# Kernel optimization log

Hardware: AMD Instinct MI355X
Metric: run time of the kernel (lower is better)

The kernel has to match this reference:

```python
import jax, jax.numpy as jnp
import numpy as np
import math

B, T, D, H, QS, VS, V, HID = 4096, 16, 32, 4, 64, 64, 65, 2048


def _sinusoidal(block_size, dmodel):
    pe = np.zeros((block_size, dmodel), dtype=np.float32)
    pos = np.arange(block_size)[:, None].astype(np.float32)
    i = np.arange(dmodel // 2).astype(np.float32)
    denom = 10000.0 ** (2.0 * i / dmodel)
    pe[:, 0::2] = np.sin(pos / denom)
    pe[:, 1::2] = np.cos(pos / denom)
    return jnp.asarray(pe)


def setup_inputs() -> dict:
    key = jax.random.key(0)
    ks = jax.random.split(key, 20)
    n = lambda k, s: jax.random.normal(k, s, jnp.float32) * 0.05
    return {
        "x": jax.random.randint(ks[0], (B, T), 0, V, dtype=jnp.int32),
        "emb": n(ks[1], (V, D)),
        "pos": _sinusoidal(T, D),
        "Wq": n(ks[2], (2, H, D, QS)), "bq": n(ks[3], (2, H, QS)),
        "Wk": n(ks[4], (2, H, D, QS)), "bk": n(ks[5], (2, H, QS)),
        "Wv": n(ks[6], (2, H, D, VS)), "bv": n(ks[7], (2, H, VS)),
        "Wo": n(ks[8], (2, H * VS, D)), "bo": n(ks[9], (2, D)),
        "ga": jnp.ones((2, D), jnp.float32), "ba": jnp.zeros((2, D), jnp.float32),
        "W1": n(ks[10], (2, D, HID)), "b1": n(ks[11], (2, HID)),
        "W2": n(ks[12], (2, HID, D)), "b2": n(ks[13], (2, D)),
        "gm": jnp.ones((2, D), jnp.float32), "bm": jnp.zeros((2, D), jnp.float32),
        "Wf": n(ks[14], (D, V)), "bf": n(ks[15], (V,)),
    }


def _ln(x, g, b, eps=1e-5):
    m = jnp.mean(x, axis=-1, keepdims=True)
    v = jnp.mean((x - m) ** 2, axis=-1, keepdims=True)
    return (x - m) * jax.lax.rsqrt(v + eps) * g + b


def reference(x, emb, pos, Wq, bq, Wk, bk, Wv, bv, Wo, bo, ga, ba,
              W1, b1, W2, b2, gm, bm, Wf, bf):
    # embed + sinusoidal pos, scaled by sqrt(dmodel) (as in source)
    h = (emb[x] + pos) * math.sqrt(D)  # [B,T,D]
    mask = jnp.tril(jnp.ones((T, T), dtype=bool))
    for l in range(2):
        # all H heads at once: [B,H,T,QS]
        q = jnp.einsum('btd,hdq->bhtq', h, Wq[l]) + bq[l][:, None, :]
        k = jnp.einsum('btd,hdq->bhtq', h, Wk[l]) + bk[l][:, None, :]
        v = jnp.einsum('btd,hdv->bhtv', h, Wv[l]) + bv[l][:, None, :]
        s = jnp.einsum('bhtq,bhsq->bhts', q, k) / math.sqrt(QS)
        s = jnp.where(mask, s, -jnp.inf)
        a = jax.nn.softmax(s, axis=-1)
        o = jnp.einsum('bhts,bhsv->bhtv', a, v)
        o = o.transpose(0, 2, 1, 3).reshape(h.shape[0], T, H * VS)  # concat heads
        o = o @ Wo[l] + bo[l]
        h = _ln(o + h, ga[l], ba[l])
        m = jax.nn.relu(h @ W1[l] + b1[l]) @ W2[l] + b2[l]
        h = _ln(h + m, gm[l], bm[l])
    return h @ Wf + bf  # logits [B,T,V]
```

## Files before the change

kernel.cpp:

```cpp
#include <hip/hip_runtime.h>

typedef __bf16 bf16;
typedef __bf16 bf16x4 __attribute__((ext_vector_type(4)));
typedef __bf16 bf16x8 __attribute__((ext_vector_type(8)));
typedef short  s16x4  __attribute__((ext_vector_type(4)));
typedef float  f32x4  __attribute__((ext_vector_type(4)));

#define VOC 65

#define LDS_FENCE() asm volatile("s_waitcnt lgkmcnt(0)" ::: "memory")

#define WS_WQ 0
#define WS_WK 16384
#define WS_WV 32768
#define WS_WO 49152
#define WS_W1 65536
#define WS_W2 196608
#define WS_WF 327680

__global__ void transpose_f32bf16_k(const float* __restrict__ src, bf16* __restrict__ dst,
                                    int batch, int R, int C) {
  int i = blockIdx.x * blockDim.x + threadIdx.x;
  int total = batch * R * C;
  if (i >= total) return;
  int b = i / (R * C);
  int rc = i - b * (R * C);
  int r = rc / C;
  int c = rc - r * C;
  dst[(b * C + c) * R + r] = (bf16)src[i];
}

__global__ void prep_wf_k(const float* __restrict__ wf, bf16* __restrict__ dst) {
  int i = blockIdx.x * blockDim.x + threadIdx.x;
  if (i >= 80 * 32) return;
  int c = i >> 5, r = i & 31;
  dst[i] = (c < VOC) ? (bf16)wf[r * VOC + c] : (bf16)0.0f;
}


#define MFMA32(a,b,c) __builtin_amdgcn_mfma_f32_16x16x32_bf16((a),(b),(c),0,0,0)

static __device__ __forceinline__ f32x4 MFMA16(bf16x4 a, bf16x4 b, f32x4 c) {
  return __builtin_amdgcn_mfma_f32_16x16x16bf16_1k(
      __builtin_bit_cast(s16x4, a), __builtin_bit_cast(s16x4, b), c, 0, 0, 0);
}

static __device__ __forceinline__ f32x4 splat4(float v) {
  f32x4 s; s[0] = v; s[1] = v; s[2] = v; s[3] = v; return s;
}

#define NS 4

__global__ __launch_bounds__(128)
void xformer_k(const int* __restrict__ x, const float* __restrict__ emb, const float* __restrict__ pos,
               const float* __restrict__ bq, const float* __restrict__ bk, const float* __restrict__ bv,
               const float* __restrict__ bo, const float* __restrict__ ga, const float* __restrict__ ba,
               const float* __restrict__ b1, const float* __restrict__ b2,
               const float* __restrict__ gm, const float* __restrict__ bm,
               const float* __restrict__ bfin,
               const bf16* __restrict__ ws, float* __restrict__ out)
{
  __shared__ bf16 hbnc[2][NS][16][40];
  const int tid  = threadIdx.x;
  const int wv   = tid >> 6;
  const int lane = tid & 63;
  const int lo   = lane & 15;
  const int hi   = lane >> 4;
  const int seq0 = blockIdx.x * (2*NS) + wv * NS;

  const bf16* wqT = ws + WS_WQ;
  const bf16* wkT = ws + WS_WK;
  const bf16* wvT = ws + WS_WV;
  const bf16* woT = ws + WS_WO;
  const bf16* w1T = ws + WS_W1;
  const bf16* w2T = ws + WS_W2;
  const bf16* wfT = ws + WS_WF;

  const f32x4 fz = {0.f, 0.f, 0.f, 0.f};

  bf16x8 bh[NS];
  bf16x4 hD0[NS], hD1[NS];

  #pragma unroll
  for (int si = 0; si < NS; ++si) {
    const int s = seq0 + si;
    int idl = x[s*16 + lo];
    idl = idl < 0 ? 0 : (idl >= VOC ? VOC - 1 : idl);
    f32x4 e0 = *(const f32x4*)(emb + idl*32 + hi*8);
    f32x4 e1 = *(const f32x4*)(emb + idl*32 + hi*8 + 4);
    f32x4 p0 = *(const f32x4*)(pos + lo*32 + hi*8);
    f32x4 p1 = *(const f32x4*)(pos + lo*32 + hi*8 + 4);
    bf16x8 hv;
    #pragma unroll
    for (int j = 0; j < 4; ++j) {
      hv[j]   = (bf16)((e0[j] + p0[j]) * 5.656854249492381f);
      hv[4+j] = (bf16)((e1[j] + p1[j]) * 5.656854249492381f);
    }
    bh[si] = hv;
    bf16x4 d0, d1;
    #pragma unroll
    for (int r = 0; r < 4; ++r) {
      int tr = hi*4 + r;
      int idr = x[s*16 + tr];
      idr = idr < 0 ? 0 : (idr >= VOC ? VOC - 1 : idr);
      d0[r] = (bf16)((emb[idr*32 + lo]      + pos[tr*32 + lo])      * 5.656854249492381f);
      d1[r] = (bf16)((emb[idr*32 + 16 + lo] + pos[tr*32 + 16 + lo]) * 5.656854249492381f);
    }
    hD0[si] = d0; hD1[si] = d1;
  }

  for (int l = 0; l < 2; ++l) {
    f32x4 accO[NS][2];
    {
      float bo0 = bo[l*32 + lo], bo1 = bo[l*32 + 16 + lo];
      #pragma unroll
      for (int si = 0; si < NS; ++si) { accO[si][0] = splat4(bo0); accO[si][1] = splat4(bo1); }
    }
    #pragma unroll
    for (int hh = 0; hh < 4; ++hh) {
      const int hb = (l*4 + hh) * 64;
      f32x4 sf[NS];
      #pragma unroll
      for (int si = 0; si < NS; ++si) sf[si] = fz;
      #pragma unroll
      for (int nt = 0; nt < 4; ++nt) {
        const int wofs = (hb + nt*16 + lo)*32 + hi*8;
        bf16x8 wq8 = *(const bf16x8*)(wqT + wofs);
        bf16x8 wk8 = *(const bf16x8*)(wkT + wofs);
        f32x4 bq4 = *(const f32x4*)(bq + hb + nt*16 + hi*4);
        f32x4 bk4 = *(const f32x4*)(bk + hb + nt*16 + hi*4);
        #pragma unroll
        for (int si = 0; si < NS; ++si) {
          f32x4 dq = MFMA32(wq8, bh[si], bq4);
          f32x4 dk = MFMA32(wk8, bh[si], bk4);
          bf16x4 pq, pk;
          #pragma unroll
          for (int r = 0; r < 4; ++r) {
            pq[r] = (bf16)dq[r];
            pk[r] = (bf16)dk[r];
          }
          sf[si] = MFMA16(pk, pq, sf[si]);
        }
      }
      bf16x4 pp[NS];
      #pragma unroll
      for (int si = 0; si < NS; ++si) {
        float e[4], mx = -3.0e4f, sm = 0.f;
        #pragma unroll
        for (int r = 0; r < 4; ++r) {
          int key = hi*4 + r;
          e[r] = (key <= lo) ? sf[si][r] * 0.125f : -3.0e4f;
          mx = fmaxf(mx, e[r]);
        }
        mx = fmaxf(mx, __shfl_xor(mx, 16));
        mx = fmaxf(mx, __shfl_xor(mx, 32));
        #pragma unroll
        for (int r = 0; r < 4; ++r) { e[r] = __expf(e[r] - mx); sm += e[r]; }
        sm += __shfl_xor(sm, 16);
        sm += __shfl_xor(sm, 32);
        float inv = 1.0f / sm;
        bf16x4 p4;
        #pragma unroll
        for (int r = 0; r < 4; ++r) p4[r] = (bf16)(e[r] * inv);
        pp[si] = p4;
      }
      #pragma unroll
      for (int nt = 0; nt < 4; ++nt) {
        bf16x8 wv8 = *(const bf16x8*)(wvT + (hb + nt*16 + lo)*32 + hi*8);
        f32x4 bv4 = splat4(bv[hb + nt*16 + lo]);
        bf16x4 wo4[2];
        #pragma unroll
        for (int n2 = 0; n2 < 2; ++n2)
          wo4[n2] = *(const bf16x4*)(woT + (l*32 + n2*16 + lo)*256 + hh*64 + nt*16 + hi*4);
        #pragma unroll
        for (int si = 0; si < NS; ++si) {
          f32x4 dv = MFMA32(bh[si], wv8, bv4);
          bf16x4 vz;
          #pragma unroll
          for (int r = 0; r < 4; ++r) vz[r] = (bf16)dv[r];
          f32x4 o = MFMA16(vz, pp[si], fz);
          bf16x4 oz;
          #pragma unroll
          for (int r = 0; r < 4; ++r) oz[r] = (bf16)o[r];
          #pragma unroll
          for (int n2 = 0; n2 < 2; ++n2)
            accO[si][n2] = MFMA16(oz, wo4[n2], accO[si][n2]);
        }
      }
    }
    {
      float g0 = ga[l*32 + lo], g1 = ga[l*32 + 16 + lo];
      float a0 = ba[l*32 + lo], a1 = ba[l*32 + 16 + lo];
      #pragma unroll
      for (int si = 0; si < NS; ++si) {
        bf16x4 nh0, nh1;
        #pragma unroll
        for (int r = 0; r < 4; ++r) {
          float v0 = accO[si][0][r] + (float)hD0[si][r];
          float v1 = accO[si][1][r] + (float)hD1[si][r];
          float s1 = v0 + v1, s2 = v0*v0 + v1*v1;
          s1 += __shfl_xor(s1, 1); s2 += __shfl_xor(s2, 1);
          s1 += __shfl_xor(s1, 2); s2 += __shfl_xor(s2, 2);
          s1 += __shfl_xor(s1, 4); s2 += __shfl_xor(s2, 4);
          s1 += __shfl_xor(s1, 8); s2 += __shfl_xor(s2, 8);
          float mean = s1 * (1.f/32.f);
          float var  = s2 * (1.f/32.f) - mean*mean;
          float rs   = rsqrtf(fabsf(var) + 1e-5f);
          float h0 = (v0 - mean)*rs*g0 + a0;
          float h1 = (v1 - mean)*rs*g1 + a1;
          nh0[r] = (bf16)h0; nh1[r] = (bf16)h1;
          hbnc[wv][si][hi*4 + r][lo]      = (bf16)h0;
          hbnc[wv][si][hi*4 + r][16 + lo] = (bf16)h1;
        }
        hD0[si] = nh0; hD1[si] = nh1;
      }
      LDS_FENCE();
      #pragma unroll
      for (int si = 0; si < NS; ++si)
        bh[si] = *(const bf16x8*)(&hbnc[wv][si][lo][hi*8]);
      LDS_FENCE();
    }
    f32x4 acc2[NS][2];
    {
      float b20 = b2[l*32 + lo], b21 = b2[l*32 + 16 + lo];
      #pragma unroll
      for (int si = 0; si < NS; ++si) { acc2[si][0] = splat4(b20); acc2[si][1] = splat4(b21); }
    }
    const bf16* w1l = w1T + l*65536;
    const bf16* w2l = w2T + l*65536;
    const float* b1l = b1 + l*2048;
    bf16x8 A1[2]; bf16x4 A2[2][2]; f32x4 Ab[2];
    bf16x8 B1[2]; bf16x4 B2[2][2]; f32x4 Bb[2];
    #pragma unroll
    for (int c = 0; c < 2; ++c) {
      A1[c] = *(const bf16x8*)(w1l + (c*16 + lo)*32 + hi*8);
      Ab[c] = *(const f32x4*)(b1l + c*16 + hi*4);
      B1[c] = *(const bf16x8*)(w1l + (32 + c*16 + lo)*32 + hi*8);
      Bb[c] = *(const f32x4*)(b1l + 32 + c*16 + hi*4);
      #pragma unroll
      for (int n2 = 0; n2 < 2; ++n2) {
        A2[c][n2] = *(const bf16x4*)(w2l + (n2*16 + lo)*2048 + c*16 + hi*4);
        B2[c][n2] = *(const bf16x4*)(w2l + (n2*16 + lo)*2048 + 32 + c*16 + hi*4);
      }
    }
    for (int kk = 0; kk < 64; kk += 2) {
      {
        const int k2 = ((kk + 2) & 63) * 32;
        bf16x8 n1[2]; bf16x4 n2v[2][2]; f32x4 nb[2];
        #pragma unroll
        for (int c = 0; c < 2; ++c) {
          n1[c] = *(const bf16x8*)(w1l + (k2 + c*16 + lo)*32 + hi*8);
          nb[c] = *(const f32x4*)(b1l + k2 + c*16 + hi*4);
          #pragma unroll
          for (int n2 = 0; n2 < 2; ++n2)
            n2v[c][n2] = *(const bf16x4*)(w2l + (n2*16 + lo)*2048 + k2 + c*16 + hi*4);
        }
        #pragma unroll
        for (int c = 0; c < 2; ++c) {
          #pragma unroll
          for (int si = 0; si < NS; ++si) {
            f32x4 d = MFMA32(A1[c], bh[si], Ab[c]);
            bf16x4 mz;
            #pragma unroll
            for (int r = 0; r < 4; ++r) mz[r] = (bf16)fmaxf(d[r], 0.f);
            acc2[si][0] = MFMA16(mz, A2[c][0], acc2[si][0]);
            acc2[si][1] = MFMA16(mz, A2[c][1], acc2[si][1]);
          }
        }
        #pragma unroll
        for (int c = 0; c < 2; ++c) {
          A1[c] = n1[c]; Ab[c] = nb[c];
          A2[c][0] = n2v[c][0]; A2[c][1] = n2v[c][1];
        }
      }
      {
        const int k3 = ((kk + 3) & 63) * 32;
        bf16x8 n1[2]; bf16x4 n2v[2][2]; f32x4 nb[2];
        #pragma unroll
        for (int c = 0; c < 2; ++c) {
          n1[c] = *(const bf16x8*)(w1l + (k3 + c*16 + lo)*32 + hi*8);
          nb[c] = *(const f32x4*)(b1l + k3 + c*16 + hi*4);
          #pragma unroll
          for (int n2 = 0; n2 < 2; ++n2)
            n2v[c][n2] = *(const bf16x4*)(w2l + (n2*16 + lo)*2048 + k3 + c*16 + hi*4);
        }
        #pragma unroll
        for (int c = 0; c < 2; ++c) {
          #pragma unroll
          for (int si = 0; si < NS; ++si) {
            f32x4 d = MFMA32(B1[c], bh[si], Bb[c]);
            bf16x4 mz;
            #pragma unroll
            for (int r = 0; r < 4; ++r) mz[r] = (bf16)fmaxf(d[r], 0.f);
            acc2[si][0] = MFMA16(mz, B2[c][0], acc2[si][0]);
            acc2[si][1] = MFMA16(mz, B2[c][1], acc2[si][1]);
          }
        }
        #pragma unroll
        for (int c = 0; c < 2; ++c) {
          B1[c] = n1[c]; Bb[c] = nb[c];
          B2[c][0] = n2v[c][0]; B2[c][1] = n2v[c][1];
        }
      }
    }
    {
      float g0 = gm[l*32 + lo], g1 = gm[l*32 + 16 + lo];
      float a0 = bm[l*32 + lo], a1 = bm[l*32 + 16 + lo];
      #pragma unroll
      for (int si = 0; si < NS; ++si) {
        bf16x4 nh0, nh1;
        #pragma unroll
        for (int r = 0; r < 4; ++r) {
          float v0 = acc2[si][0][r] + (float)hD0[si][r];
          float v1 = acc2[si][1][r] + (float)hD1[si][r];
          float s1 = v0 + v1, s2 = v0*v0 + v1*v1;
          s1 += __shfl_xor(s1, 1); s2 += __shfl_xor(s2, 1);
          s1 += __shfl_xor(s1, 2); s2 += __shfl_xor(s2, 2);
          s1 += __shfl_xor(s1, 4); s2 += __shfl_xor(s2, 4);
          s1 += __shfl_xor(s1, 8); s2 += __shfl_xor(s2, 8);
          float mean = s1 * (1.f/32.f);
          float var  = s2 * (1.f/32.f) - mean*mean;
          float rs   = rsqrtf(fabsf(var) + 1e-5f);
          float h0 = (v0 - mean)*rs*g0 + a0;
          float h1 = (v1 - mean)*rs*g1 + a1;
          nh0[r] = (bf16)h0; nh1[r] = (bf16)h1;
          hbnc[wv][si][hi*4 + r][lo]      = (bf16)h0;
          hbnc[wv][si][hi*4 + r][16 + lo] = (bf16)h1;
        }
        hD0[si] = nh0; hD1[si] = nh1;
      }
      LDS_FENCE();
      #pragma unroll
      for (int si = 0; si < NS; ++si)
        bh[si] = *(const bf16x8*)(&hbnc[wv][si][lo][hi*8]);
      LDS_FENCE();
    }
  }

  #pragma unroll
  for (int si = 0; si < NS; ++si) {
    const int s = seq0 + si;
    bf16x8 a = bh[si];
    #pragma unroll
    for (int nt = 0; nt < 5; ++nt) {
      int col = nt*16 + lo;
      f32x4 cb = splat4((col < VOC) ? bfin[col] : 0.f);
      bf16x8 w = *(const bf16x8*)(wfT + (nt*16 + lo)*32 + hi*8);
      f32x4 d = MFMA32(a, w, cb);
      if (col < VOC) {
        #pragma unroll
        for (int r = 0; r < 4; ++r)
          out[(s*16 + hi*4 + r)*VOC + col] = d[r];
      }
    }
  }
}

extern "C" void kernel_launch(void* const* d_in, const int* in_sizes, int n_in,
                              void* d_out, int out_size, void* d_ws, size_t ws_size,
                              hipStream_t stream) {
  const int*   x   = (const int*)d_in[0];
  const float* emb = (const float*)d_in[1];
  const float* pos = (const float*)d_in[2];
  const float* Wq  = (const float*)d_in[3];
  const float* bq  = (const float*)d_in[4];
  const float* Wk  = (const float*)d_in[5];
  const float* bk  = (const float*)d_in[6];
  const float* Wv  = (const float*)d_in[7];
  const float* bv  = (const float*)d_in[8];
  const float* Wo  = (const float*)d_in[9];
  const float* bo  = (const float*)d_in[10];
  const float* ga  = (const float*)d_in[11];
  const float* ba  = (const float*)d_in[12];
  const float* W1  = (const float*)d_in[13];
  const float* b1  = (const float*)d_in[14];
  const float* W2  = (const float*)d_in[15];
  const float* b2  = (const float*)d_in[16];
  const float* gm  = (const float*)d_in[17];
  const float* bm  = (const float*)d_in[18];
  const float* Wf  = (const float*)d_in[19];
  const float* bfin= (const float*)d_in[20];

  bf16* ws = (bf16*)d_ws;

  transpose_f32bf16_k<<<64, 256, 0, stream>>>(Wq, ws + WS_WQ, 8, 32, 64);
  transpose_f32bf16_k<<<64, 256, 0, stream>>>(Wk, ws + WS_WK, 8, 32, 64);
  transpose_f32bf16_k<<<64, 256, 0, stream>>>(Wv, ws + WS_WV, 8, 32, 64);
  transpose_f32bf16_k<<<64, 256, 0, stream>>>(Wo, ws + WS_WO, 2, 256, 32);
  transpose_f32bf16_k<<<512, 256, 0, stream>>>(W1, ws + WS_W1, 2, 32, 2048);
  transpose_f32bf16_k<<<512, 256, 0, stream>>>(W2, ws + WS_W2, 2, 2048, 32);
  prep_wf_k<<<10, 256, 0, stream>>>(Wf, ws + WS_WF);

  xformer_k<<<512, 128, 0, stream>>>(x, emb, pos, bq, bk, bv, bo, ga, ba,
                                     b1, b2, gm, bm, bfin,
                                     ws, (float*)d_out);
}
```

Baseline: 145.2 us.

## Use K=32 MFMA for QK scores and FFN down-projection with permuted W2

```diff
diff --git a/kernel.cpp b/kernel.cpp
--- a/kernel.cpp
+++ b/kernel.cpp
@@ -30,6 +30,19 @@
   dst[(b * C + c) * R + r] = (bf16)src[i];
 }
 
+__global__ void prep_w2perm_k(const float* __restrict__ src, bf16* __restrict__ dst) {
+  int i = blockIdx.x * blockDim.x + threadIdx.x;
+  if (i >= 2 * 2048 * 32) return;
+  int l   = i >> 16;
+  int rem = i & 65535;
+  int hid = rem >> 5;
+  int out = rem & 31;
+  int h5 = hid & 31;
+  int c  = (h5 >> 4) & 1, hh = (h5 >> 2) & 3, r = h5 & 3;
+  int hid_p = (hid & ~31) | (hh << 3) | (c << 2) | r;
+  dst[(l*32 + out)*2048 + hid_p] = (bf16)src[i];
+}
+
 __global__ void prep_wf_k(const float* __restrict__ wf, bf16* __restrict__ dst) {
   int i = blockIdx.x * blockDim.x + threadIdx.x;
   if (i >= 80 * 32) return;
@@ -50,6 +63,25 @@
 }
 
 #define NS 4
+
+struct FSet {
+  bf16x8 w10, w11;
+  bf16x8 w20, w21;
+  f32x4  b0, b1;
+};
+
+static __device__ __forceinline__ FSet load_fset(const bf16* w1l, const bf16* w2l,
+                                                 const float* b1l, int kk, int lo, int hi) {
+  FSet S;
+  const int hb = (kk & 63) * 32;
+  S.w10 = *(const bf16x8*)(w1l + (hb + lo)*32 + hi*8);
+  S.w11 = *(const bf16x8*)(w1l + (hb + 16 + lo)*32 + hi*8);
+  S.b0  = *(const f32x4*)(b1l + hb + hi*4);
+  S.b1  = *(const f32x4*)(b1l + hb + 16 + hi*4);
+  S.w20 = *(const bf16x8*)(w2l + (lo)*2048 + hb + hi*8);
+  S.w21 = *(const bf16x8*)(w2l + (16 + lo)*2048 + hb + hi*8);
+  return S;
+}
 
 __global__ __launch_bounds__(128)
 void xformer_k(const int* __restrict__ x, const float* __restrict__ emb, const float* __restrict__ pos,
@@ -123,24 +155,30 @@
       #pragma unroll
       for (int si = 0; si < NS; ++si) sf[si] = fz;
       #pragma unroll
-      for (int nt = 0; nt < 4; ++nt) {
-        const int wofs = (hb + nt*16 + lo)*32 + hi*8;
-        bf16x8 wq8 = *(const bf16x8*)(wqT + wofs);
-        bf16x8 wk8 = *(const bf16x8*)(wkT + wofs);
-        f32x4 bq4 = *(const f32x4*)(bq + hb + nt*16 + hi*4);
-        f32x4 bk4 = *(const f32x4*)(bk + hb + nt*16 + hi*4);
-        #pragma unroll
-        for (int si = 0; si < NS; ++si) {
-          f32x4 dq = MFMA32(wq8, bh[si], bq4);
-          f32x4 dk = MFMA32(wk8, bh[si], bk4);
-          bf16x4 pq, pk;
+      for (int ntp = 0; ntp < 2; ++ntp) {
+        bf16x8 pq8[NS], pk8[NS];
+        #pragma unroll
+        for (int c = 0; c < 2; ++c) {
+          const int nt = ntp*2 + c;
+          const int wofs = (hb + nt*16 + lo)*32 + hi*8;
+          bf16x8 wq8 = *(const bf16x8*)(wqT + wofs);
+          bf16x8 wk8 = *(const bf16x8*)(wkT + wofs);
+          f32x4 bq4 = *(const f32x4*)(bq + hb + nt*16 + hi*4);
+          f32x4 bk4 = *(const f32x4*)(bk + hb + nt*16 + hi*4);
           #pragma unroll
-          for (int r = 0; r < 4; ++r) {
-            pq[r] = (bf16)dq[r];
-            pk[r] = (bf16)dk[r];
+          for (int si = 0; si < NS; ++si) {
+            f32x4 dq = MFMA32(wq8, bh[si], bq4);
+            f32x4 dk = MFMA32(wk8, bh[si], bk4);
+            #pragma unroll
+            for (int r = 0; r < 4; ++r) {
+              pq8[si][c*4 + r] = (bf16)dq[r];
+              pk8[si][c*4 + r] = (bf16)dk[r];
+            }
           }
-          sf[si] = MFMA16(pk, pq, sf[si]);
-        }
+        }
+        #pragma unroll
+        for (int si = 0; si < NS; ++si)
+          sf[si] = MFMA32(pk8[si], pq8[si], sf[si]);
       }
       bf16x4 pp[NS];
       #pragma unroll
@@ -229,79 +267,25 @@
     const bf16* w1l = w1T + l*65536;
     const bf16* w2l = w2T + l*65536;
     const float* b1l = b1 + l*2048;
-    bf16x8 A1[2]; bf16x4 A2[2][2]; f32x4 Ab[2];
-    bf16x8 B1[2]; bf16x4 B2[2][2]; f32x4 Bb[2];
-    #pragma unroll
-    for (int c = 0; c < 2; ++c) {
-      A1[c] = *(const bf16x8*)(w1l + (c*16 + lo)*32 + hi*8);
-      Ab[c] = *(const f32x4*)(b1l + c*16 + hi*4);
-      B1[c] = *(const bf16x8*)(w1l + (32 + c*16 + lo)*32 + hi*8);
-      Bb[c] = *(const f32x4*)(b1l + 32 + c*16 + hi*4);
-      #pragma unroll
-      for (int n2 = 0; n2 < 2; ++n2) {
-        A2[c][n2] = *(const bf16x4*)(w2l + (n2*16 + lo)*2048 + c*16 + hi*4);
-        B2[c][n2] = *(const bf16x4*)(w2l + (n2*16 + lo)*2048 + 32 + c*16 + hi*4);
-      }
-    }
-    for (int kk = 0; kk < 64; kk += 2) {
-      {
-        const int k2 = ((kk + 2) & 63) * 32;
-        bf16x8 n1[2]; bf16x4 n2v[2][2]; f32x4 nb[2];
-        #pragma unroll
-        for (int c = 0; c < 2; ++c) {
-          n1[c] = *(const bf16x8*)(w1l + (k2 + c*16 + lo)*32 + hi*8);
-          nb[c] = *(const f32x4*)(b1l + k2 + c*16 + hi*4);
-          #pragma unroll
-          for (int n2 = 0; n2 < 2; ++n2)
-            n2v[c][n2] = *(const bf16x4*)(w2l + (n2*16 + lo)*2048 + k2 + c*16 + hi*4);
-        }
-        #pragma unroll
-        for (int c = 0; c < 2; ++c) {
-          #pragma unroll
-          for (int si = 0; si < NS; ++si) {
-            f32x4 d = MFMA32(A1[c], bh[si], Ab[c]);
-            bf16x4 mz;
-            #pragma unroll
-            for (int r = 0; r < 4; ++r) mz[r] = (bf16)fmaxf(d[r], 0.f);
-            acc2[si][0] = MFMA16(mz, A2[c][0], acc2[si][0]);
-            acc2[si][1] = MFMA16(mz, A2[c][1], acc2[si][1]);
-          }
-        }
-        #pragma unroll
-        for (int c = 0; c < 2; ++c) {
-          A1[c] = n1[c]; Ab[c] = nb[c];
-          A2[c][0] = n2v[c][0]; A2[c][1] = n2v[c][1];
-        }
-      }
-      {
-        const int k3 = ((kk + 3) & 63) * 32;
-        bf16x8 n1[2]; bf16x4 n2v[2][2]; f32x4 nb[2];
-        #pragma unroll
-        for (int c = 0; c < 2; ++c) {
-          n1[c] = *(const bf16x8*)(w1l + (k3 + c*16 + lo)*32 + hi*8);
-          nb[c] = *(const f32x4*)(b1l + k3 + c*16 + hi*4);
-          #pragma unroll
-          for (int n2 = 0; n2 < 2; ++n2)
-            n2v[c][n2] = *(const bf16x4*)(w2l + (n2*16 + lo)*2048 + k3 + c*16 + hi*4);
-        }
-        #pragma unroll
-        for (int c = 0; c < 2; ++c) {
-          #pragma unroll
-          for (int si = 0; si < NS; ++si) {
-            f32x4 d = MFMA32(B1[c], bh[si], Bb[c]);
-            bf16x4 mz;
-            #pragma unroll
-            for (int r = 0; r < 4; ++r) mz[r] = (bf16)fmaxf(d[r], 0.f);
-            acc2[si][0] = MFMA16(mz, B2[c][0], acc2[si][0]);
-            acc2[si][1] = MFMA16(mz, B2[c][1], acc2[si][1]);
-          }
-        }
-        #pragma unroll
-        for (int c = 0; c < 2; ++c) {
-          B1[c] = n1[c]; Bb[c] = nb[c];
-          B2[c][0] = n2v[c][0]; B2[c][1] = n2v[c][1];
-        }
-      }
+    FSet SA = load_fset(w1l, w2l, b1l, 0, lo, hi);
+    FSet SB = load_fset(w1l, w2l, b1l, 1, lo, hi);
+    #pragma unroll 2
+    for (int kk = 0; kk < 64; ++kk) {
+      FSet N = load_fset(w1l, w2l, b1l, kk + 2, lo, hi);
+      #pragma unroll
+      for (int si = 0; si < NS; ++si) {
+        f32x4 d0 = MFMA32(SA.w10, bh[si], SA.b0);
+        f32x4 d1 = MFMA32(SA.w11, bh[si], SA.b1);
+        bf16x8 m8;
+        #pragma unroll
+        for (int r = 0; r < 4; ++r) {
+          m8[r]     = (bf16)fmaxf(d0[r], 0.f);
+          m8[4 + r] = (bf16)fmaxf(d1[r], 0.f);
+        }
+        acc2[si][0] = MFMA32(m8, SA.w20, acc2[si][0]);
+        acc2[si][1] = MFMA32(m8, SA.w21, acc2[si][1]);
+      }
+      SA = SB; SB = N;
     }
     {
       float g0 = gm[l*32 + lo], g1 = gm[l*32 + 16 + lo];
@@ -388,7 +372,7 @@
   transpose_f32bf16_k<<<64, 256, 0, stream>>>(Wv, ws + WS_WV, 8, 32, 64);
   transpose_f32bf16_k<<<64, 256, 0, stream>>>(Wo, ws + WS_WO, 2, 256, 32);
   transpose_f32bf16_k<<<512, 256, 0, stream>>>(W1, ws + WS_W1, 2, 32, 2048);
-  transpose_f32bf16_k<<<512, 256, 0, stream>>>(W2, ws + WS_W2, 2, 2048, 32);
+  prep_w2perm_k<<<512, 256, 0, stream>>>(W2, ws + WS_W2);
   prep_wf_k<<<10, 256, 0, stream>>>(Wf, ws + WS_WF);
 
   xformer_k<<<512, 128, 0, stream>>>(x, emb, pos, bq, bk, bv, bo, ga, ba,
```

Measured after the change: 160.7 us. 1.11x slower.
